# Optimization experiments

Measured on AMD Instinct MI355X. Metric: run time of the kernel, lower is better.

Reference implementation:

```python
import jax, jax.numpy as jnp
import numpy as np

NPOINT = 2048
NSAMPLE = 16
LEAKY = 0.1
BN_EPS = 1e-5


def square_distance(src, dst):
    # src [B,S,3], dst [B,N,3] -> [B,S,N] squared euclidean
    d = -2.0 * jnp.einsum('bsc,bnc->bsn', src, dst)
    d = d + jnp.sum(src * src, -1)[:, :, None]
    d = d + jnp.sum(dst * dst, -1)[:, None, :]
    return d


def furthest_point_sample(xyz, npoint):
    # xyz [B,N,3] -> idx [B,npoint]; matches pointnet2 CUDA (seed = index 0)
    B, N, _ = xyz.shape

    def step(carry, _):
        dist, far = carry  # dist [B,N], far [B]
        centroid = jnp.take_along_axis(xyz, far[:, None, None], axis=1)  # [B,1,3]
        d = jnp.sum((xyz - centroid) ** 2, axis=-1)
        dist = jnp.minimum(dist, d)
        nxt = jnp.argmax(dist, axis=-1).astype(jnp.int32)
        return (dist, nxt), far

    init = (jnp.full((B, N), 1e10, xyz.dtype), jnp.zeros((B,), jnp.int32))
    _, idxs = jax.lax.scan(step, init, None, length=npoint)
    return idxs.T  # [B, npoint]


def _gather_nbrs(p, i):
    # p [N,C], i [S,K] -> [S,K,C]
    return p[i]


gather_group = jax.vmap(_gather_nbrs)


def conv_bn_lrelu(x, W, g, b):
    # x [B,Cin,S,K], W [Cout,Cin]; 1x1 conv + train-mode BatchNorm2d + LeakyReLU
    y = jnp.einsum('oc,bcsk->bosk', W, x)
    mean = jnp.mean(y, axis=(0, 2, 3), keepdims=True)
    var = jnp.var(y, axis=(0, 2, 3), keepdims=True)
    y = (y - mean) * jax.lax.rsqrt(var + BN_EPS)
    y = y * g[None, :, None, None] + b[None, :, None, None]
    return jnp.where(y > 0, y, LEAKY * y)


def setup_inputs() -> dict:
    key = jax.random.key(0)
    ks = jax.random.split(key, 5)
    B, N, D = 4, 8192, 64
    return {
        'xyz': jax.random.normal(ks[0], (B, 3, N), jnp.float32),
        'points': jax.random.normal(ks[1], (B, D, N), jnp.float32),
        'conv0_w': jax.random.normal(ks[2], (64, 67), jnp.float32) * 0.05,
        'conv1_w': jax.random.normal(ks[3], (64, 64), jnp.float32) * 0.05,
        'conv2_w': jax.random.normal(ks[4], (128, 64), jnp.float32) * 0.05,
        'bn0_g': jnp.ones((64,), jnp.float32),
        'bn0_b': jnp.zeros((64,), jnp.float32),
        'bn1_g': jnp.ones((64,), jnp.float32),
        'bn1_b': jnp.zeros((64,), jnp.float32),
        'bn2_g': jnp.ones((128,), jnp.float32),
        'bn2_b': jnp.zeros((128,), jnp.float32),
    }


def reference(xyz, points, conv0_w, conv1_w, conv2_w,
              bn0_g, bn0_b, bn1_g, bn1_b, bn2_g, bn2_b):
    xyz_t = jnp.transpose(xyz, (0, 2, 1))      # [B,N,3]
    pts_t = jnp.transpose(points, (0, 2, 1))   # [B,N,D]

    fps_idx = furthest_point_sample(xyz_t, NPOINT)                       # [B,S]
    new_xyz = jnp.take_along_axis(xyz_t, fps_idx[:, :, None], axis=1)    # [B,S,3]

    sqrd = square_distance(new_xyz, xyz_t)                               # [B,S,N]
    _, idx = jax.lax.top_k(-sqrd, NSAMPLE)                               # [B,S,K]

    grouped_xyz = gather_group(xyz_t, idx)                               # [B,S,K,3]
    grouped_norm = grouped_xyz - new_xyz[:, :, None, :]
    grouped_pts = gather_group(pts_t, idx)                               # [B,S,K,D]
    new_points = jnp.concatenate([grouped_norm, grouped_pts], axis=-1)   # [B,S,K,D+3]
    new_points = jnp.transpose(new_points, (0, 3, 1, 2))                 # [B,D+3,S,K]

    for W, g, b in ((conv0_w, bn0_g, bn0_b), (conv1_w, bn1_g, bn1_b),
                    (conv2_w, bn2_g, bn2_b)):
        new_points = conv_bn_lrelu(new_points, W, g, b)

    feat = jnp.max(new_points, axis=-1)                                  # [B,128,S]
    return jnp.transpose(new_xyz, (0, 2, 1)), feat, fps_idx
```

## Files before the change

### kernel.cpp

```cpp
#include <hip/hip_runtime.h>
#include <hip/hip_bf16.h>

#define BB 4
#define NP 8192
#define SS 2048
#define KK 16
#define DD 64
#define NN (BB*SS*KK)
#define HEATERS 128

typedef float vf2 __attribute__((ext_vector_type(2)));

#if defined(__has_builtin)
#if __has_builtin(__builtin_amdgcn_permlane16_swap) && __has_builtin(__builtin_amdgcn_permlane32_swap)
#define HAVE_PERMLANE_SWAP 1
#endif
#endif

__device__ __forceinline__ float wave_max_f32(float v) {
  int x;
  x = __builtin_amdgcn_update_dpp(0, __float_as_int(v), 0xB1, 0xF, 0xF, true);
  v = fmaxf(v, __int_as_float(x));
  x = __builtin_amdgcn_update_dpp(0, __float_as_int(v), 0x4E, 0xF, 0xF, true);
  v = fmaxf(v, __int_as_float(x));
  x = __builtin_amdgcn_update_dpp(0, __float_as_int(v), 0x141, 0xF, 0xF, true);
  v = fmaxf(v, __int_as_float(x));
  x = __builtin_amdgcn_update_dpp(0, __float_as_int(v), 0x140, 0xF, 0xF, true);
  v = fmaxf(v, __int_as_float(x));
#ifdef HAVE_PERMLANE_SWAP
  {
    unsigned u = __float_as_uint(v);
    auto r16 = __builtin_amdgcn_permlane16_swap(u, u, false, false);
    v = fmaxf(__uint_as_float(r16[0]), __uint_as_float(r16[1]));
    unsigned u2 = __float_as_uint(v);
    auto r32 = __builtin_amdgcn_permlane32_swap(u2, u2, false, false);
    v = fmaxf(__uint_as_float(r32[0]), __uint_as_float(r32[1]));
  }
#else
  x = __builtin_amdgcn_ds_swizzle(__float_as_int(v), 0x401F);
  v = fmaxf(v, __int_as_float(x));
  v = fmaxf(v, __shfl_xor(v, 32, 64));
#endif
  return v;
}

__global__ __launch_bounds__(512) void fps_kernel(
    const float* __restrict__ xyz, float* __restrict__ newXyz,
    float* __restrict__ out, int* __restrict__ done)
{
  const int t = threadIdx.x;

  if (blockIdx.x >= BB) {
    float a0 = 1.0f, a1 = 1.1f, a2 = 1.2f, a3 = 1.3f;
    const float bm = 1.000001f, cm = 1e-7f;
    for (;;) {
      for (int k = 0; k < 1024; k++) {
        a0 = __builtin_fmaf(a0, bm, cm);
        a1 = __builtin_fmaf(a1, bm, cm);
        a2 = __builtin_fmaf(a2, bm, cm);
        a3 = __builtin_fmaf(a3, bm, cm);
      }
      if (__hip_atomic_load(done, __ATOMIC_RELAXED, __HIP_MEMORY_SCOPE_AGENT) >= BB)
        break;
    }
    if (a0 == 123.456f && a1 == 2.f && a2 == 3.f && a3 == 4.f)
      ((volatile int*)done)[1] = 1;
    return;
  }

  const int b = blockIdx.x;
  const float* xb = xyz + (size_t)b * 3 * NP;

  __shared__ float lx[NP], ly[NP], lz[NP];
  __shared__ int   wis[SS];
  __shared__ unsigned long long swin[3];

  vf2 px[8], py[8], pz[8], dist[8];
  const int i0 = t << 4;
#pragma unroll
  for (int h = 0; h < 8; h++) {
    int i = i0 + (h << 1);
    vf2 x = *(const vf2*)(xb + i);
    vf2 y = *(const vf2*)(xb + NP + i);
    vf2 z = *(const vf2*)(xb + 2 * NP + i);
    px[h] = x; py[h] = y; pz[h] = z;
    dist[h] = (vf2){1e10f, 1e10f};
    *(vf2*)(lx + i) = x; *(vf2*)(ly + i) = y; *(vf2*)(lz + i) = z;
  }
  if (t == 0) { wis[0] = 0; swin[0] = 0; swin[1] = 0; swin[2] = 0; }
  __syncthreads();

  float cx = lx[0], cy = ly[0], cz = lz[0];

  for (int it = 1; it < SS; ++it) {
    vf2 c2x = {cx, cx}, c2y = {cy, cy}, c2z = {cz, cz};
    vf2 lb = {-1.0f, -1.0f};
    {
#pragma clang fp contract(off)
#pragma unroll
      for (int h = 0; h < 8; h++) {
        vf2 dx = px[h] - c2x;
        vf2 dy = py[h] - c2y;
        vf2 dz = pz[h] - c2z;
        vf2 d  = (dx * dx + dy * dy) + dz * dz;
        vf2 dm = __builtin_elementwise_min(dist[h], d);
        dist[h] = dm;
        lb = __builtin_elementwise_max(lb, dm);
      }
    }
    float lbest = fmaxf(lb.x, lb.y);
    float Vw = wave_max_f32(lbest);
    int q = it % 3;
    if (lbest == Vw) {
      unsigned mi = 0u;
#pragma unroll
      for (int h = 7; h >= 0; h--) {
        unsigned base = (unsigned)(i0 + (h << 1));
        if (dist[h].y == Vw) mi = base + 1;
        if (dist[h].x == Vw) mi = base;
      }
      unsigned long long pk =
          ((unsigned long long)__float_as_uint(Vw) << 32) | (unsigned)(~mi);
      atomicMax(&swin[q], pk);
    }
    __syncthreads();
    unsigned long long pkf = swin[q];
    int ii = (int)(~((unsigned)pkf));
    if (t == 0) { wis[it] = ii; swin[(q + 2) % 3] = 0; }
    cx = lx[ii]; cy = ly[ii]; cz = lz[ii];
  }
  __syncthreads();

  float* outX = out;
  float* outI = out + 24576 + 1048576;
  for (int s = t; s < SS; s += 512) {
    int iw = wis[s];
    float x = lx[iw], y = ly[iw], z = lz[iw];
    size_t qq = (size_t)(b * SS + s);
    newXyz[qq * 3 + 0] = x;
    newXyz[qq * 3 + 1] = y;
    newXyz[qq * 3 + 2] = z;
    outX[(b * 3 + 0) * SS + s] = x;
    outX[(b * 3 + 1) * SS + s] = y;
    outX[(b * 3 + 2) * SS + s] = z;
    outI[b * SS + s] = (float)iw;
  }
  if (t == 0)
    __hip_atomic_fetch_add(done, 1, __ATOMIC_RELEASE, __HIP_MEMORY_SCOPE_AGENT);
}

__global__ __launch_bounds__(256) void knn_kernel(
    const float* __restrict__ xyz, const float* __restrict__ newXyz,
    int* __restrict__ knnIdx)
{
  const int t = threadIdx.x, w = t >> 6, l = t & 63;
  const int q = blockIdx.x * 4 + w;
  const int b = q >> 11;
  const float* xb = xyz + (size_t)b * 3 * NP;
  float qx = newXyz[q * 3], qy = newXyz[q * 3 + 1], qz = newXyz[q * 3 + 2];
  float ss = __fadd_rn(__fadd_rn(__fmul_rn(qx, qx), __fmul_rn(qy, qy)), __fmul_rn(qz, qz));
  float kd[16]; int ki[16];
#pragma unroll
  for (int j = 0; j < 16; j++) { kd[j] = __builtin_inff(); ki[j] = 0x7fffffff; }

  for (int m = 0; m < 32; m++) {
    int i = (m << 8) + (l << 2);
    float4 xv = *(const float4*)(xb + i);
    float4 yv = *(const float4*)(xb + NP + i);
    float4 zv = *(const float4*)(xb + 2 * NP + i);
#pragma unroll
    for (int c = 0; c < 4; c++) {
      float x = (c == 0) ? xv.x : (c == 1) ? xv.y : (c == 2) ? xv.z : xv.w;
      float y = (c == 0) ? yv.x : (c == 1) ? yv.y : (c == 2) ? yv.z : yv.w;
      float z = (c == 0) ? zv.x : (c == 1) ? zv.y : (c == 2) ? zv.z : zv.w;
      float dot = __fadd_rn(__fadd_rn(__fmul_rn(x, qx), __fmul_rn(y, qy)), __fmul_rn(z, qz));
      float nn  = __fadd_rn(__fadd_rn(__fmul_rn(x, x), __fmul_rn(y, y)), __fmul_rn(z, z));
      float d   = __fadd_rn(__fadd_rn(__fmul_rn(-2.0f, dot), ss), nn);
      if (d < kd[15]) {
        kd[15] = d; ki[15] = i + c;
#pragma unroll
        for (int jj = 15; jj >= 1; jj--) {
          if (kd[jj] < kd[jj - 1]) {
            float td = kd[jj]; kd[jj] = kd[jj - 1]; kd[jj - 1] = td;
            int   ti = ki[jj]; ki[jj] = ki[jj - 1]; ki[jj - 1] = ti;
          }
        }
      }
    }
  }

  __shared__ float sd[4 * 64 * 17];
  __shared__ int   sx[4 * 64 * 17];
  int base = (w * 64 + l) * 17;
#pragma unroll
  for (int j = 0; j < 16; j++) { sd[base + j] = kd[j]; sx[base + j] = ki[j]; }
  __syncthreads();

  int cur = 0; int outIdx = 0;
#pragma unroll 1
  for (int r = 0; r < 16; r++) {
    float hv = (cur < 16) ? sd[base + cur] : __builtin_inff();
    int   hi = (cur < 16) ? sx[base + cur] : 0x7fffffff;
    int   hl = l;
#pragma unroll
    for (int m2 = 1; m2 < 64; m2 <<= 1) {
      float ov = __shfl_xor(hv, m2, 64);
      int   oi = __shfl_xor(hi, m2, 64);
      int   ol = __shfl_xor(hl, m2, 64);
      if (ov < hv || (ov == hv && oi < hi)) { hv = ov; hi = oi; hl = ol; }
    }
    if (l == hl) cur++;
    if (l == r) outIdx = hi;
  }
  if (l < 16) knnIdx[q * 16 + l] = outIdx;
}

__global__ __launch_bounds__(256) void conv0_kernel(
    const float* __restrict__ xyz, const float* __restrict__ points,
    const float* __restrict__ newXyz, const int* __restrict__ knnIdx,
    const float* __restrict__ W, float* __restrict__ Y)
{
  int n = blockIdx.x * 256 + threadIdx.x;
  int b = n >> 15;
  int q = n >> 4;
  int ip = knnIdx[n];
  const float* xb = xyz + (size_t)b * 3 * NP;
  float x[67];
  x[0] = xb[ip]          - newXyz[q * 3 + 0];
  x[1] = xb[NP + ip]     - newXyz[q * 3 + 1];
  x[2] = xb[2 * NP + ip] - newXyz[q * 3 + 2];
  const float* pb = points + (size_t)b * DD * NP + ip;
#pragma unroll 8
  for (int d0 = 0; d0 < DD; d0++)
    x[3 + d0] = pb[(size_t)d0 * NP];
#pragma unroll 1
  for (int o = 0; o < 64; o += 4) {
    float a0 = 0.f, a1 = 0.f, a2 = 0.f, a3 = 0.f;
#pragma unroll
    for (int c = 0; c < 67; c++) {
      float xv = x[c];
      a0 = fmaf(W[(o + 0) * 67 + c], xv, a0);
      a1 = fmaf(W[(o + 1) * 67 + c], xv, a1);
      a2 = fmaf(W[(o + 2) * 67 + c], xv, a2);
      a3 = fmaf(W[(o + 3) * 67 + c], xv, a3);
    }
    Y[(size_t)(o + 0) * NN + n] = a0;
    Y[(size_t)(o + 1) * NN + n] = a1;
    Y[(size_t)(o + 2) * NN + n] = a2;
    Y[(size_t)(o + 3) * NN + n] = a3;
  }
}

template <int CIN, int COUT>
__global__ __launch_bounds__(256) void conv_bn_kernel(
    const float* __restrict__ X, const float* __restrict__ W,
    const float* __restrict__ stats, const float* __restrict__ g,
    const float* __restrict__ bt, float* __restrict__ Y)
{
  __shared__ vf2 sss[CIN];
  if (threadIdx.x < CIN) {
    int c = threadIdx.x;
    float mean = stats[c * 2] * (1.0f / NN);
    float var  = stats[c * 2 + 1] * (1.0f / NN) - mean * mean;
    float inv  = rsqrtf(var + 1e-5f);
    float sc = inv * g[c];
    float sh = bt[c] - mean * sc;
    sss[c] = (vf2){sc, sh};
  }
  __syncthreads();
  int n = blockIdx.x * 256 + threadIdx.x;
  float x[CIN];
#pragma unroll
  for (int c = 0; c < CIN; c++) x[c] = X[(size_t)c * NN + n];
#pragma unroll
  for (int c = 0; c < CIN; c++) {
    vf2 p = sss[c];
    float v = fmaf(x[c], p.x, p.y);
    x[c] = v > 0.0f ? v : 0.1f * v;
  }
#pragma unroll 1
  for (int o = 0; o < COUT; o += 4) {
    float a0 = 0.f, a1 = 0.f, a2 = 0.f, a3 = 0.f;
#pragma unroll
    for (int c = 0; c < CIN; c++) {
      float xv = x[c];
      a0 = fmaf(W[(o + 0) * CIN + c], xv, a0);
      a1 = fmaf(W[(o + 1) * CIN + c], xv, a1);
      a2 = fmaf(W[(o + 2) * CIN + c], xv, a2);
      a3 = fmaf(W[(o + 3) * CIN + c], xv, a3);
    }
    Y[(size_t)(o + 0) * NN + n] = a0;
    Y[(size_t)(o + 1) * NN + n] = a1;
    Y[(size_t)(o + 2) * NN + n] = a2;
    Y[(size_t)(o + 3) * NN + n] = a3;
  }
}

__global__ __launch_bounds__(256) void stats_kernel(
    const float* __restrict__ Y, float* __restrict__ stats)
{
  int c = blockIdx.y;
  int base = blockIdx.x * 4096 + threadIdx.x;
  const float* yc = Y + (size_t)c * NN;
  float s1 = 0.f, s2 = 0.f;
#pragma unroll
  for (int j = 0; j < 16; j++) {
    float v = yc[base + j * 256];
    s1 += v; s2 = fmaf(v, v, s2);
  }
#pragma unroll
  for (int m = 1; m < 64; m <<= 1) {
    s1 += __shfl_xor(s1, m, 64);
    s2 += __shfl_xor(s2, m, 64);
  }
  __shared__ float r1[4], r2[4];
  int w = threadIdx.x >> 6;
  if ((threadIdx.x & 63) == 0) { r1[w] = s1; r2[w] = s2; }
  __syncthreads();
  if (threadIdx.x == 0) {
    float t1 = r1[0] + r1[1] + r1[2] + r1[3];
    float t2 = r2[0] + r2[1] + r2[2] + r2[3];
    atomicAdd(&stats[c * 2], t1);
    atomicAdd(&stats[c * 2 + 1], t2);
  }
}

__global__ __launch_bounds__(256) void maxk_kernel(
    const float* __restrict__ X, const float* __restrict__ stats,
    const float* __restrict__ g, const float* __restrict__ bt,
    float* __restrict__ out)
{
  int m = blockIdx.x * 256 + threadIdx.x;
  int s = m & 2047;
  int o = (m >> 11) & 127;
  int b = m >> 18;
  float mean = stats[o * 2] * (1.0f / NN);
  float var  = stats[o * 2 + 1] * (1.0f / NN) - mean * mean;
  float inv  = rsqrtf(var + 1e-5f);
  float sc = inv * g[o];
  float sh = bt[o] - mean * sc;
  const float4* p = (const float4*)(X + (size_t)o * NN + ((size_t)((b << 11) + s) << 4));
  float mx = -__builtin_inff();
#pragma unroll
  for (int j = 0; j < 4; j++) {
    float4 v4 = p[j];
    float a = fmaf(v4.x, sc, sh); a = a > 0.f ? a : 0.1f * a;
    float b2 = fmaf(v4.y, sc, sh); b2 = b2 > 0.f ? b2 : 0.1f * b2;
    float c = fmaf(v4.z, sc, sh); c = c > 0.f ? c : 0.1f * c;
    float d = fmaf(v4.w, sc, sh); d = d > 0.f ? d : 0.1f * d;
    mx = fmaxf(mx, fmaxf(fmaxf(a, b2), fmaxf(c, d)));
  }
  out[24576 + (size_t)((b << 7) + o) * SS + s] = mx;
}

extern "C" void kernel_launch(void* const* d_in, const int* in_sizes, int n_in,
                              void* d_out, int out_size, void* d_ws, size_t ws_size,
                              hipStream_t stream) {
  const float* xyz    = (const float*)d_in[0];
  const float* points = (const float*)d_in[1];
  const float* w0 = (const float*)d_in[2];
  const float* w1 = (const float*)d_in[3];
  const float* w2 = (const float*)d_in[4];
  const float* g0 = (const float*)d_in[5];
  const float* b0 = (const float*)d_in[6];
  const float* g1 = (const float*)d_in[7];
  const float* b1 = (const float*)d_in[8];
  const float* g2 = (const float*)d_in[9];
  const float* b2 = (const float*)d_in[10];
  float* out = (float*)d_out;

  float* wsf    = (float*)d_ws;
  float* newXyz = wsf;
  int*   knnIdx = (int*)(wsf + 24576);
  float* stats0 = wsf + 155648;
  float* stats1 = wsf + 155904;
  float* stats2 = wsf + 156160;
  int*   done   = (int*)(wsf + 157440);
  float* Xa     = wsf + 160000;
  float* Xb     = wsf + 8941824;

  hipMemsetAsync(stats0, 0, 2048 * 4, stream);

  fps_kernel<<<BB + HEATERS, 512, 0, stream>>>(xyz, newXyz, out, done);
  knn_kernel<<<SS * BB / 4, 256, 0, stream>>>(xyz, newXyz, knnIdx);

  conv0_kernel<<<NN / 256, 256, 0, stream>>>(xyz, points, newXyz, knnIdx, w0, Xb);
  stats_kernel<<<dim3(32, 64), 256, 0, stream>>>(Xb, stats0);

  conv_bn_kernel<64, 64><<<NN / 256, 256, 0, stream>>>(Xb, w1, stats0, g0, b0, Xa);
  stats_kernel<<<dim3(32, 64), 256, 0, stream>>>(Xa, stats1);

  conv_bn_kernel<64, 128><<<NN / 256, 256, 0, stream>>>(Xa, w2, stats1, g1, b1, Xb);
  stats_kernel<<<dim3(32, 128), 256, 0, stream>>>(Xb, stats2);

  maxk_kernel<<<(BB * 128 * SS) / 256, 256, 0, stream>>>(Xb, stats2, g2, b2, out);
}
```

Measured before the change: 2.285 ms.

## Overlap KNN with FPS by streaming centroids to spinning worker blocks

The idle heater blocks in the FPS launch become KNN workers. The FPS blocks publish each new centroid to global memory with atomic stores as soon as it is chosen. Workers spin on sentinel-initialised slots, which are set to 0xFF by a memset, and run the top-16 search for each query while FPS is still iterating. This removes the separate KNN kernel launch and hides its cost behind the serial FPS chain. The risks are spin-wait dependence on co-residency of all blocks and extra per-iteration global stores in the FPS critical loop.

```diff
diff --git a/kernel.cpp b/kernel.cpp
--- a/kernel.cpp
+++ b/kernel.cpp
@@ -7,7 +7,7 @@
 #define KK 16
 #define DD 64
 #define NN (BB*SS*KK)
-#define HEATERS 128
+#define WORKERS 251
 
 typedef float vf2 __attribute__((ext_vector_type(2)));
 
@@ -44,36 +44,127 @@
   return v;
 }
 
+#define SENT 0xFFFFFFFFu
+
 __global__ __launch_bounds__(512) void fps_kernel(
     const float* __restrict__ xyz, float* __restrict__ newXyz,
-    float* __restrict__ out, int* __restrict__ done)
+    float* __restrict__ out, int* __restrict__ done, int* __restrict__ knnIdx)
 {
+  __shared__ __align__(16) char smem[106528];
   const int t = threadIdx.x;
 
   if (blockIdx.x >= BB) {
+    const int w = t >> 6, l = t & 63;
+    float* sd = (float*)smem;
+    int*   sx = (int*)(smem + 34816);
+    const int base = (w * 64 + l) * 17;
+    float hacc = 0.0f;
+    const unsigned gw = (blockIdx.x - BB) * 8 + (unsigned)w;
+
+    for (unsigned q = gw; q < (unsigned)(BB * SS); q += WORKERS * 8) {
+      const int b = q >> 11;
+      const float* xb = xyz + (size_t)b * 3 * NP;
+      const unsigned* nxz = (const unsigned*)newXyz + (size_t)q * 3;
+      float qx, qy, qz;
+      {
+        float h0 = 1.0f, h1 = 1.1f, h2 = 1.2f, h3 = 1.3f;
+        for (;;) {
+          unsigned ux = __hip_atomic_load(nxz + 0, __ATOMIC_RELAXED, __HIP_MEMORY_SCOPE_AGENT);
+          unsigned uy = __hip_atomic_load(nxz + 1, __ATOMIC_RELAXED, __HIP_MEMORY_SCOPE_AGENT);
+          unsigned uz = __hip_atomic_load(nxz + 2, __ATOMIC_RELAXED, __HIP_MEMORY_SCOPE_AGENT);
+          if (ux != SENT && uy != SENT && uz != SENT) {
+            qx = __uint_as_float(ux); qy = __uint_as_float(uy); qz = __uint_as_float(uz);
+            break;
+          }
+#pragma unroll
+          for (int k2 = 0; k2 < 16; k2++) {
+            h0 = __builtin_fmaf(h0, 1.000001f, 1e-7f);
+            h1 = __builtin_fmaf(h1, 1.000001f, 1e-7f);
+            h2 = __builtin_fmaf(h2, 1.000001f, 1e-7f);
+            h3 = __builtin_fmaf(h3, 1.000001f, 1e-7f);
+          }
+        }
+        hacc += h0 + h1 + h2 + h3;
+      }
+
+      float ssq = __fadd_rn(__fadd_rn(__fmul_rn(qx, qx), __fmul_rn(qy, qy)), __fmul_rn(qz, qz));
+      float kd[16]; int ki[16];
+#pragma unroll
+      for (int j = 0; j < 16; j++) { kd[j] = __builtin_inff(); ki[j] = 0x7fffffff; }
+
+      for (int m = 0; m < 32; m++) {
+        int i = (m << 8) + (l << 2);
+        float4 xv = *(const float4*)(xb + i);
+        float4 yv = *(const float4*)(xb + NP + i);
+        float4 zv = *(const float4*)(xb + 2 * NP + i);
+#pragma unroll
+        for (int c = 0; c < 4; c++) {
+          float x = (c == 0) ? xv.x : (c == 1) ? xv.y : (c == 2) ? xv.z : xv.w;
+          float y = (c == 0) ? yv.x : (c == 1) ? yv.y : (c == 2) ? yv.z : yv.w;
+          float z = (c == 0) ? zv.x : (c == 1) ? zv.y : (c == 2) ? zv.z : zv.w;
+          float dot = __fadd_rn(__fadd_rn(__fmul_rn(x, qx), __fmul_rn(y, qy)), __fmul_rn(z, qz));
+          float nn  = __fadd_rn(__fadd_rn(__fmul_rn(x, x), __fmul_rn(y, y)), __fmul_rn(z, z));
+          float d   = __fadd_rn(__fadd_rn(__fmul_rn(-2.0f, dot), ssq), nn);
+          if (d < kd[15]) {
+            kd[15] = d; ki[15] = i + c;
+#pragma unroll
+            for (int jj = 15; jj >= 1; jj--) {
+              if (kd[jj] < kd[jj - 1]) {
+                float td = kd[jj]; kd[jj] = kd[jj - 1]; kd[jj - 1] = td;
+                int   ti = ki[jj]; ki[jj] = ki[jj - 1]; ki[jj - 1] = ti;
+              }
+            }
+          }
+        }
+      }
+
+#pragma unroll
+      for (int j = 0; j < 16; j++) { sd[base + j] = kd[j]; sx[base + j] = ki[j]; }
+
+      int cur = 0; int outIdx = 0;
+#pragma unroll 1
+      for (int r = 0; r < 16; r++) {
+        float hv = (cur < 16) ? sd[base + cur] : __builtin_inff();
+        int   hi = (cur < 16) ? sx[base + cur] : 0x7fffffff;
+        int   hl = l;
+#pragma unroll
+        for (int m2 = 1; m2 < 64; m2 <<= 1) {
+          float ov = __shfl_xor(hv, m2, 64);
+          int   oi = __shfl_xor(hi, m2, 64);
+          int   ol = __shfl_xor(hl, m2, 64);
+          if (ov < hv || (ov == hv && oi < hi)) { hv = ov; hi = oi; hl = ol; }
+        }
+        if (l == hl) cur++;
+        if (l == r) outIdx = hi;
+      }
+      if (l < 16) knnIdx[q * 16 + l] = outIdx;
+    }
+
     float a0 = 1.0f, a1 = 1.1f, a2 = 1.2f, a3 = 1.3f;
-    const float bm = 1.000001f, cm = 1e-7f;
     for (;;) {
       for (int k = 0; k < 1024; k++) {
-        a0 = __builtin_fmaf(a0, bm, cm);
-        a1 = __builtin_fmaf(a1, bm, cm);
-        a2 = __builtin_fmaf(a2, bm, cm);
-        a3 = __builtin_fmaf(a3, bm, cm);
+        a0 = __builtin_fmaf(a0, 1.000001f, 1e-7f);
+        a1 = __builtin_fmaf(a1, 1.000001f, 1e-7f);
+        a2 = __builtin_fmaf(a2, 1.000001f, 1e-7f);
+        a3 = __builtin_fmaf(a3, 1.000001f, 1e-7f);
       }
       if (__hip_atomic_load(done, __ATOMIC_RELAXED, __HIP_MEMORY_SCOPE_AGENT) >= BB)
         break;
     }
-    if (a0 == 123.456f && a1 == 2.f && a2 == 3.f && a3 == 4.f)
+    if (hacc + a0 + a1 + a2 + a3 == 123.456f)
       ((volatile int*)done)[1] = 1;
     return;
   }
 
+  float* lx = (float*)smem;
+  float* ly = (float*)(smem + 32768);
+  float* lz = (float*)(smem + 65536);
+  int*   wis = (int*)(smem + 98304);
+  unsigned long long* swin = (unsigned long long*)(smem + 106496);
+
   const int b = blockIdx.x;
   const float* xb = xyz + (size_t)b * 3 * NP;
-
-  __shared__ float lx[NP], ly[NP], lz[NP];
-  __shared__ int   wis[SS];
-  __shared__ unsigned long long swin[3];
+  unsigned* nxzOut = (unsigned*)newXyz + (size_t)b * SS * 3;
 
   vf2 px[8], py[8], pz[8], dist[8];
   const int i0 = t << 4;
@@ -91,6 +182,11 @@
   __syncthreads();
 
   float cx = lx[0], cy = ly[0], cz = lz[0];
+  if (t == 0) {
+    __hip_atomic_store(nxzOut + 0, __float_as_uint(cx), __ATOMIC_RELAXED, __HIP_MEMORY_SCOPE_AGENT);
+    __hip_atomic_store(nxzOut + 1, __float_as_uint(cy), __ATOMIC_RELAXED, __HIP_MEMORY_SCOPE_AGENT);
+    __hip_atomic_store(nxzOut + 2, __float_as_uint(cz), __ATOMIC_RELAXED, __HIP_MEMORY_SCOPE_AGENT);
+  }
 
   for (int it = 1; it < SS; ++it) {
     vf2 c2x = {cx, cx}, c2y = {cy, cy}, c2z = {cz, cz};
@@ -128,6 +224,12 @@
     int ii = (int)(~((unsigned)pkf));
     if (t == 0) { wis[it] = ii; swin[(q + 2) % 3] = 0; }
     cx = lx[ii]; cy = ly[ii]; cz = lz[ii];
+    if (t == 0) {
+      unsigned* nx = nxzOut + (size_t)it * 3;
+      __hip_atomic_store(nx + 0, __float_as_uint(cx), __ATOMIC_RELAXED, __HIP_MEMORY_SCOPE_AGENT);
+      __hip_atomic_store(nx + 1, __float_as_uint(cy), __ATOMIC_RELAXED, __HIP_MEMORY_SCOPE_AGENT);
+      __hip_atomic_store(nx + 2, __float_as_uint(cz), __ATOMIC_RELAXED, __HIP_MEMORY_SCOPE_AGENT);
+    }
   }
   __syncthreads();
 
@@ -135,84 +237,13 @@
   float* outI = out + 24576 + 1048576;
   for (int s = t; s < SS; s += 512) {
     int iw = wis[s];
-    float x = lx[iw], y = ly[iw], z = lz[iw];
-    size_t qq = (size_t)(b * SS + s);
-    newXyz[qq * 3 + 0] = x;
-    newXyz[qq * 3 + 1] = y;
-    newXyz[qq * 3 + 2] = z;
-    outX[(b * 3 + 0) * SS + s] = x;
-    outX[(b * 3 + 1) * SS + s] = y;
-    outX[(b * 3 + 2) * SS + s] = z;
+    outX[(b * 3 + 0) * SS + s] = lx[iw];
+    outX[(b * 3 + 1) * SS + s] = ly[iw];
+    outX[(b * 3 + 2) * SS + s] = lz[iw];
     outI[b * SS + s] = (float)iw;
   }
   if (t == 0)
     __hip_atomic_fetch_add(done, 1, __ATOMIC_RELEASE, __HIP_MEMORY_SCOPE_AGENT);
-}
-
-__global__ __launch_bounds__(256) void knn_kernel(
-    const float* __restrict__ xyz, const float* __restrict__ newXyz,
-    int* __restrict__ knnIdx)
-{
-  const int t = threadIdx.x, w = t >> 6, l = t & 63;
-  const int q = blockIdx.x * 4 + w;
-  const int b = q >> 11;
-  const float* xb = xyz + (size_t)b * 3 * NP;
-  float qx = newXyz[q * 3], qy = newXyz[q * 3 + 1], qz = newXyz[q * 3 + 2];
-  float ss = __fadd_rn(__fadd_rn(__fmul_rn(qx, qx), __fmul_rn(qy, qy)), __fmul_rn(qz, qz));
-  float kd[16]; int ki[16];
-#pragma unroll
-  for (int j = 0; j < 16; j++) { kd[j] = __builtin_inff(); ki[j] = 0x7fffffff; }
-
-  for (int m = 0; m < 32; m++) {
-    int i = (m << 8) + (l << 2);
-    float4 xv = *(const float4*)(xb + i);
-    float4 yv = *(const float4*)(xb + NP + i);
-    float4 zv = *(const float4*)(xb + 2 * NP + i);
-#pragma unroll
-    for (int c = 0; c < 4; c++) {
-      float x = (c == 0) ? xv.x : (c == 1) ? xv.y : (c == 2) ? xv.z : xv.w;
-      float y = (c == 0) ? yv.x : (c == 1) ? yv.y : (c == 2) ? yv.z : yv.w;
-      float z = (c == 0) ? zv.x : (c == 1) ? zv.y : (c == 2) ? zv.z : zv.w;
-      float dot = __fadd_rn(__fadd_rn(__fmul_rn(x, qx), __fmul_rn(y, qy)), __fmul_rn(z, qz));
-      float nn  = __fadd_rn(__fadd_rn(__fmul_rn(x, x), __fmul_rn(y, y)), __fmul_rn(z, z));
-      float d   = __fadd_rn(__fadd_rn(__fmul_rn(-2.0f, dot), ss), nn);
-      if (d < kd[15]) {
-        kd[15] = d; ki[15] = i + c;
-#pragma unroll
-        for (int jj = 15; jj >= 1; jj--) {
-          if (kd[jj] < kd[jj - 1]) {
-            float td = kd[jj]; kd[jj] = kd[jj - 1]; kd[jj - 1] = td;
-            int   ti = ki[jj]; ki[jj] = ki[jj - 1]; ki[jj - 1] = ti;
-          }
-        }
-      }
-    }
-  }
-
-  __shared__ float sd[4 * 64 * 17];
-  __shared__ int   sx[4 * 64 * 17];
-  int base = (w * 64 + l) * 17;
-#pragma unroll
-  for (int j = 0; j < 16; j++) { sd[base + j] = kd[j]; sx[base + j] = ki[j]; }
-  __syncthreads();
-
-  int cur = 0; int outIdx = 0;
-#pragma unroll 1
-  for (int r = 0; r < 16; r++) {
-    float hv = (cur < 16) ? sd[base + cur] : __builtin_inff();
-    int   hi = (cur < 16) ? sx[base + cur] : 0x7fffffff;
-    int   hl = l;
-#pragma unroll
-    for (int m2 = 1; m2 < 64; m2 <<= 1) {
-      float ov = __shfl_xor(hv, m2, 64);
-      int   oi = __shfl_xor(hi, m2, 64);
-      int   ol = __shfl_xor(hl, m2, 64);
-      if (ov < hv || (ov == hv && oi < hi)) { hv = ov; hi = oi; hl = ol; }
-    }
-    if (l == hl) cur++;
-    if (l == r) outIdx = hi;
-  }
-  if (l < 16) knnIdx[q * 16 + l] = outIdx;
 }
 
 __global__ __launch_bounds__(256) void conv0_kernel(
@@ -380,9 +411,9 @@
   float* Xb     = wsf + 8941824;
 
   hipMemsetAsync(stats0, 0, 2048 * 4, stream);
-
-  fps_kernel<<<BB + HEATERS, 512, 0, stream>>>(xyz, newXyz, out, done);
-  knn_kernel<<<SS * BB / 4, 256, 0, stream>>>(xyz, newXyz, knnIdx);
+  hipMemsetAsync(newXyz, 0xFF, 24576 * 4, stream);
+
+  fps_kernel<<<BB + WORKERS, 512, 0, stream>>>(xyz, newXyz, out, done, knnIdx);
 
   conv0_kernel<<<NN / 256, 256, 0, stream>>>(xyz, points, newXyz, knnIdx, w0, Xb);
   stats_kernel<<<dim3(32, 64), 256, 0, stream>>>(Xb, stats0);
```

Result: slower. 2.534 ms (+10.9%).

## Fuse conv/BN/stats/maxpool tail into one persistent kernel with grid barriers

Applied to the files above, without the earlier changes.

Replaces the seven separate conv, stats and max-pool launches with a single persistent kernel of 512 blocks. A global atomic-counter barrier separates the phases. This is meant to remove launch gaps and kernel boundaries between the dependent stages. It relies on all 512 blocks being co-resident to avoid deadlock, and it adds spin-wait barrier cost.

```diff
diff --git a/kernel.cpp b/kernel.cpp
--- a/kernel.cpp
+++ b/kernel.cpp
@@ -8,6 +8,7 @@
 #define DD 64
 #define NN (BB*SS*KK)
 #define HEATERS 128
+#define TB 512
 
 typedef float vf2 __attribute__((ext_vector_type(2)));
 
@@ -215,142 +216,253 @@
   if (l < 16) knnIdx[q * 16 + l] = outIdx;
 }
 
-__global__ __launch_bounds__(256) void conv0_kernel(
+__device__ __forceinline__ void gbar(int* ctr, int target) {
+  __syncthreads();
+  __threadfence();
+  if (threadIdx.x == 0) {
+    __hip_atomic_fetch_add(ctr, 1, __ATOMIC_RELEASE, __HIP_MEMORY_SCOPE_AGENT);
+    while (__hip_atomic_load(ctr, __ATOMIC_ACQUIRE, __HIP_MEMORY_SCOPE_AGENT) < target)
+      __builtin_amdgcn_s_sleep(1);
+  }
+  __syncthreads();
+  __threadfence();
+}
+
+__global__ __launch_bounds__(256) void tail_kernel(
     const float* __restrict__ xyz, const float* __restrict__ points,
     const float* __restrict__ newXyz, const int* __restrict__ knnIdx,
-    const float* __restrict__ W, float* __restrict__ Y)
+    const float* __restrict__ w0, const float* __restrict__ w1,
+    const float* __restrict__ w2,
+    const float* __restrict__ g0, const float* __restrict__ b0,
+    const float* __restrict__ g1, const float* __restrict__ b1,
+    const float* __restrict__ g2, const float* __restrict__ b2,
+    float* __restrict__ stats0, float* __restrict__ stats1,
+    float* __restrict__ stats2,
+    float* __restrict__ Xa, float* __restrict__ Xb,
+    float* __restrict__ out, int* __restrict__ ctr)
 {
-  int n = blockIdx.x * 256 + threadIdx.x;
-  int b = n >> 15;
-  int q = n >> 4;
-  int ip = knnIdx[n];
-  const float* xb = xyz + (size_t)b * 3 * NP;
-  float x[67];
-  x[0] = xb[ip]          - newXyz[q * 3 + 0];
-  x[1] = xb[NP + ip]     - newXyz[q * 3 + 1];
-  x[2] = xb[2 * NP + ip] - newXyz[q * 3 + 2];
-  const float* pb = points + (size_t)b * DD * NP + ip;
+  const int bk = blockIdx.x, t = threadIdx.x, w = t >> 6;
+  __shared__ vf2 sss[64];
+  __shared__ float r1[4], r2[4];
+
+  {
+    int n = bk * 256 + t;
+    int b = n >> 15;
+    int q = n >> 4;
+    int ip = knnIdx[n];
+    const float* xb = xyz + (size_t)b * 3 * NP;
+    float x[67];
+    x[0] = xb[ip]          - newXyz[q * 3 + 0];
+    x[1] = xb[NP + ip]     - newXyz[q * 3 + 1];
+    x[2] = xb[2 * NP + ip] - newXyz[q * 3 + 2];
+    const float* pb = points + (size_t)b * DD * NP + ip;
 #pragma unroll 8
-  for (int d0 = 0; d0 < DD; d0++)
-    x[3 + d0] = pb[(size_t)d0 * NP];
-#pragma unroll 1
-  for (int o = 0; o < 64; o += 4) {
-    float a0 = 0.f, a1 = 0.f, a2 = 0.f, a3 = 0.f;
-#pragma unroll
-    for (int c = 0; c < 67; c++) {
-      float xv = x[c];
-      a0 = fmaf(W[(o + 0) * 67 + c], xv, a0);
-      a1 = fmaf(W[(o + 1) * 67 + c], xv, a1);
-      a2 = fmaf(W[(o + 2) * 67 + c], xv, a2);
-      a3 = fmaf(W[(o + 3) * 67 + c], xv, a3);
-    }
-    Y[(size_t)(o + 0) * NN + n] = a0;
-    Y[(size_t)(o + 1) * NN + n] = a1;
-    Y[(size_t)(o + 2) * NN + n] = a2;
-    Y[(size_t)(o + 3) * NN + n] = a3;
-  }
-}
-
-template <int CIN, int COUT>
-__global__ __launch_bounds__(256) void conv_bn_kernel(
-    const float* __restrict__ X, const float* __restrict__ W,
-    const float* __restrict__ stats, const float* __restrict__ g,
-    const float* __restrict__ bt, float* __restrict__ Y)
-{
-  __shared__ vf2 sss[CIN];
-  if (threadIdx.x < CIN) {
-    int c = threadIdx.x;
-    float mean = stats[c * 2] * (1.0f / NN);
-    float var  = stats[c * 2 + 1] * (1.0f / NN) - mean * mean;
+    for (int d0 = 0; d0 < DD; d0++)
+      x[3 + d0] = pb[(size_t)d0 * NP];
+#pragma unroll 1
+    for (int o = 0; o < 64; o += 4) {
+      float a0 = 0.f, a1 = 0.f, a2 = 0.f, a3 = 0.f;
+#pragma unroll
+      for (int c = 0; c < 67; c++) {
+        float xv = x[c];
+        a0 = fmaf(w0[(o + 0) * 67 + c], xv, a0);
+        a1 = fmaf(w0[(o + 1) * 67 + c], xv, a1);
+        a2 = fmaf(w0[(o + 2) * 67 + c], xv, a2);
+        a3 = fmaf(w0[(o + 3) * 67 + c], xv, a3);
+      }
+      Xb[(size_t)(o + 0) * NN + n] = a0;
+      Xb[(size_t)(o + 1) * NN + n] = a1;
+      Xb[(size_t)(o + 2) * NN + n] = a2;
+      Xb[(size_t)(o + 3) * NN + n] = a3;
+    }
+  }
+  gbar(ctr, TB);
+
+#pragma unroll 1
+  for (int p = 0; p < 4; ++p) {
+    int vb = p * TB + bk;
+    int c = vb >> 5, xc = vb & 31;
+    const float* yc = Xb + (size_t)c * NN;
+    int base = xc * 4096 + t;
+    float s1 = 0.f, s2 = 0.f;
+#pragma unroll
+    for (int j = 0; j < 16; j++) {
+      float v = yc[base + j * 256];
+      s1 += v; s2 = fmaf(v, v, s2);
+    }
+#pragma unroll
+    for (int m = 1; m < 64; m <<= 1) {
+      s1 += __shfl_xor(s1, m, 64);
+      s2 += __shfl_xor(s2, m, 64);
+    }
+    if ((t & 63) == 0) { r1[w] = s1; r2[w] = s2; }
+    __syncthreads();
+    if (t == 0) {
+      atomicAdd(&stats0[c * 2],     r1[0] + r1[1] + r1[2] + r1[3]);
+      atomicAdd(&stats0[c * 2 + 1], r2[0] + r2[1] + r2[2] + r2[3]);
+    }
+    __syncthreads();
+  }
+  gbar(ctr, 2 * TB);
+
+  {
+    if (t < 64) {
+      int c = t;
+      float mean = stats0[c * 2] * (1.0f / NN);
+      float var  = stats0[c * 2 + 1] * (1.0f / NN) - mean * mean;
+      float inv  = rsqrtf(var + 1e-5f);
+      float sc = inv * g0[c];
+      float sh = b0[c] - mean * sc;
+      sss[c] = (vf2){sc, sh};
+    }
+    __syncthreads();
+    int n = bk * 256 + t;
+    float x[64];
+#pragma unroll
+    for (int c = 0; c < 64; c++) x[c] = Xb[(size_t)c * NN + n];
+#pragma unroll
+    for (int c = 0; c < 64; c++) {
+      vf2 pp = sss[c];
+      float v = fmaf(x[c], pp.x, pp.y);
+      x[c] = v > 0.0f ? v : 0.1f * v;
+    }
+#pragma unroll 1
+    for (int o = 0; o < 64; o += 4) {
+      float a0 = 0.f, a1 = 0.f, a2 = 0.f, a3 = 0.f;
+#pragma unroll
+      for (int c = 0; c < 64; c++) {
+        float xv = x[c];
+        a0 = fmaf(w1[(o + 0) * 64 + c], xv, a0);
+        a1 = fmaf(w1[(o + 1) * 64 + c], xv, a1);
+        a2 = fmaf(w1[(o + 2) * 64 + c], xv, a2);
+        a3 = fmaf(w1[(o + 3) * 64 + c], xv, a3);
+      }
+      Xa[(size_t)(o + 0) * NN + n] = a0;
+      Xa[(size_t)(o + 1) * NN + n] = a1;
+      Xa[(size_t)(o + 2) * NN + n] = a2;
+      Xa[(size_t)(o + 3) * NN + n] = a3;
+    }
+  }
+  gbar(ctr, 3 * TB);
+
+#pragma unroll 1
+  for (int p = 0; p < 4; ++p) {
+    int vb = p * TB + bk;
+    int c = vb >> 5, xc = vb & 31;
+    const float* yc = Xa + (size_t)c * NN;
+    int base = xc * 4096 + t;
+    float s1 = 0.f, s2 = 0.f;
+#pragma unroll
+    for (int j = 0; j < 16; j++) {
+      float v = yc[base + j * 256];
+      s1 += v; s2 = fmaf(v, v, s2);
+    }
+#pragma unroll
+    for (int m = 1; m < 64; m <<= 1) {
+      s1 += __shfl_xor(s1, m, 64);
+      s2 += __shfl_xor(s2, m, 64);
+    }
+    if ((t & 63) == 0) { r1[w] = s1; r2[w] = s2; }
+    __syncthreads();
+    if (t == 0) {
+      atomicAdd(&stats1[c * 2],     r1[0] + r1[1] + r1[2] + r1[3]);
+      atomicAdd(&stats1[c * 2 + 1], r2[0] + r2[1] + r2[2] + r2[3]);
+    }
+    __syncthreads();
+  }
+  gbar(ctr, 4 * TB);
+
+  {
+    if (t < 64) {
+      int c = t;
+      float mean = stats1[c * 2] * (1.0f / NN);
+      float var  = stats1[c * 2 + 1] * (1.0f / NN) - mean * mean;
+      float inv  = rsqrtf(var + 1e-5f);
+      float sc = inv * g1[c];
+      float sh = b1[c] - mean * sc;
+      sss[c] = (vf2){sc, sh};
+    }
+    __syncthreads();
+    int n = bk * 256 + t;
+    float x[64];
+#pragma unroll
+    for (int c = 0; c < 64; c++) x[c] = Xa[(size_t)c * NN + n];
+#pragma unroll
+    for (int c = 0; c < 64; c++) {
+      vf2 pp = sss[c];
+      float v = fmaf(x[c], pp.x, pp.y);
+      x[c] = v > 0.0f ? v : 0.1f * v;
+    }
+#pragma unroll 1
+    for (int o = 0; o < 128; o += 4) {
+      float a0 = 0.f, a1 = 0.f, a2 = 0.f, a3 = 0.f;
+#pragma unroll
+      for (int c = 0; c < 64; c++) {
+        float xv = x[c];
+        a0 = fmaf(w2[(o + 0) * 64 + c], xv, a0);
+        a1 = fmaf(w2[(o + 1) * 64 + c], xv, a1);
+        a2 = fmaf(w2[(o + 2) * 64 + c], xv, a2);
+        a3 = fmaf(w2[(o + 3) * 64 + c], xv, a3);
+      }
+      Xb[(size_t)(o + 0) * NN + n] = a0;
+      Xb[(size_t)(o + 1) * NN + n] = a1;
+      Xb[(size_t)(o + 2) * NN + n] = a2;
+      Xb[(size_t)(o + 3) * NN + n] = a3;
+    }
+  }
+  gbar(ctr, 5 * TB);
+
+#pragma unroll 1
+  for (int p = 0; p < 8; ++p) {
+    int vb = p * TB + bk;
+    int c = vb >> 5, xc = vb & 31;
+    const float* yc = Xb + (size_t)c * NN;
+    int base = xc * 4096 + t;
+    float s1 = 0.f, s2 = 0.f;
+#pragma unroll
+    for (int j = 0; j < 16; j++) {
+      float v = yc[base + j * 256];
+      s1 += v; s2 = fmaf(v, v, s2);
+    }
+#pragma unroll
+    for (int m = 1; m < 64; m <<= 1) {
+      s1 += __shfl_xor(s1, m, 64);
+      s2 += __shfl_xor(s2, m, 64);
+    }
+    if ((t & 63) == 0) { r1[w] = s1; r2[w] = s2; }
+    __syncthreads();
+    if (t == 0) {
+      atomicAdd(&stats2[c * 2],     r1[0] + r1[1] + r1[2] + r1[3]);
+      atomicAdd(&stats2[c * 2 + 1], r2[0] + r2[1] + r2[2] + r2[3]);
+    }
+    __syncthreads();
+  }
+  gbar(ctr, 6 * TB);
+
+#pragma unroll 1
+  for (int p = 0; p < 8; ++p) {
+    int m = (p * TB + bk) * 256 + t;
+    int s = m & 2047;
+    int o = (m >> 11) & 127;
+    int b = m >> 18;
+    float mean = stats2[o * 2] * (1.0f / NN);
+    float var  = stats2[o * 2 + 1] * (1.0f / NN) - mean * mean;
     float inv  = rsqrtf(var + 1e-5f);
-    float sc = inv * g[c];
-    float sh = bt[c] - mean * sc;
-    sss[c] = (vf2){sc, sh};
-  }
-  __syncthreads();
-  int n = blockIdx.x * 256 + threadIdx.x;
-  float x[CIN];
-#pragma unroll
-  for (int c = 0; c < CIN; c++) x[c] = X[(size_t)c * NN + n];
-#pragma unroll
-  for (int c = 0; c < CIN; c++) {
-    vf2 p = sss[c];
-    float v = fmaf(x[c], p.x, p.y);
-    x[c] = v > 0.0f ? v : 0.1f * v;
-  }
-#pragma unroll 1
-  for (int o = 0; o < COUT; o += 4) {
-    float a0 = 0.f, a1 = 0.f, a2 = 0.f, a3 = 0.f;
-#pragma unroll
-    for (int c = 0; c < CIN; c++) {
-      float xv = x[c];
-      a0 = fmaf(W[(o + 0) * CIN + c], xv, a0);
-      a1 = fmaf(W[(o + 1) * CIN + c], xv, a1);
-      a2 = fmaf(W[(o + 2) * CIN + c], xv, a2);
-      a3 = fmaf(W[(o + 3) * CIN + c], xv, a3);
-    }
-    Y[(size_t)(o + 0) * NN + n] = a0;
-    Y[(size_t)(o + 1) * NN + n] = a1;
-    Y[(size_t)(o + 2) * NN + n] = a2;
-    Y[(size_t)(o + 3) * NN + n] = a3;
-  }
-}
-
-__global__ __launch_bounds__(256) void stats_kernel(
-    const float* __restrict__ Y, float* __restrict__ stats)
-{
-  int c = blockIdx.y;
-  int base = blockIdx.x * 4096 + threadIdx.x;
-  const float* yc = Y + (size_t)c * NN;
-  float s1 = 0.f, s2 = 0.f;
-#pragma unroll
-  for (int j = 0; j < 16; j++) {
-    float v = yc[base + j * 256];
-    s1 += v; s2 = fmaf(v, v, s2);
-  }
-#pragma unroll
-  for (int m = 1; m < 64; m <<= 1) {
-    s1 += __shfl_xor(s1, m, 64);
-    s2 += __shfl_xor(s2, m, 64);
-  }
-  __shared__ float r1[4], r2[4];
-  int w = threadIdx.x >> 6;
-  if ((threadIdx.x & 63) == 0) { r1[w] = s1; r2[w] = s2; }
-  __syncthreads();
-  if (threadIdx.x == 0) {
-    float t1 = r1[0] + r1[1] + r1[2] + r1[3];
-    float t2 = r2[0] + r2[1] + r2[2] + r2[3];
-    atomicAdd(&stats[c * 2], t1);
-    atomicAdd(&stats[c * 2 + 1], t2);
-  }
-}
-
-__global__ __launch_bounds__(256) void maxk_kernel(
-    const float* __restrict__ X, const float* __restrict__ stats,
-    const float* __restrict__ g, const float* __restrict__ bt,
-    float* __restrict__ out)
-{
-  int m = blockIdx.x * 256 + threadIdx.x;
-  int s = m & 2047;
-  int o = (m >> 11) & 127;
-  int b = m >> 18;
-  float mean = stats[o * 2] * (1.0f / NN);
-  float var  = stats[o * 2 + 1] * (1.0f / NN) - mean * mean;
-  float inv  = rsqrtf(var + 1e-5f);
-  float sc = inv * g[o];
-  float sh = bt[o] - mean * sc;
-  const float4* p = (const float4*)(X + (size_t)o * NN + ((size_t)((b << 11) + s) << 4));
-  float mx = -__builtin_inff();
-#pragma unroll
-  for (int j = 0; j < 4; j++) {
-    float4 v4 = p[j];
-    float a = fmaf(v4.x, sc, sh); a = a > 0.f ? a : 0.1f * a;
-    float b2 = fmaf(v4.y, sc, sh); b2 = b2 > 0.f ? b2 : 0.1f * b2;
-    float c = fmaf(v4.z, sc, sh); c = c > 0.f ? c : 0.1f * c;
-    float d = fmaf(v4.w, sc, sh); d = d > 0.f ? d : 0.1f * d;
-    mx = fmaxf(mx, fmaxf(fmaxf(a, b2), fmaxf(c, d)));
-  }
-  out[24576 + (size_t)((b << 7) + o) * SS + s] = mx;
+    float sc = inv * g2[o];
+    float sh = b2[o] - mean * sc;
+    const float4* pp = (const float4*)(Xb + (size_t)o * NN + ((size_t)((b << 11) + s) << 4));
+    float mx = -__builtin_inff();
+#pragma unroll
+    for (int j = 0; j < 4; j++) {
+      float4 v4 = pp[j];
+      float a = fmaf(v4.x, sc, sh); a = a > 0.f ? a : 0.1f * a;
+      float b2v = fmaf(v4.y, sc, sh); b2v = b2v > 0.f ? b2v : 0.1f * b2v;
+      float c = fmaf(v4.z, sc, sh); c = c > 0.f ? c : 0.1f * c;
+      float d = fmaf(v4.w, sc, sh); d = d > 0.f ? d : 0.1f * d;
+      mx = fmaxf(mx, fmaxf(fmaxf(a, b2v), fmaxf(c, d)));
+    }
+    out[24576 + (size_t)((b << 7) + o) * SS + s] = mx;
+  }
 }
 
 extern "C" void kernel_launch(void* const* d_in, const int* in_sizes, int n_in,
@@ -376,6 +488,7 @@
   float* stats1 = wsf + 155904;
   float* stats2 = wsf + 156160;
   int*   done   = (int*)(wsf + 157440);
+  int*   ctr    = (int*)(wsf + 157500);
   float* Xa     = wsf + 160000;
   float* Xb     = wsf + 8941824;
 
@@ -383,15 +496,7 @@
 
   fps_kernel<<<BB + HEATERS, 512, 0, stream>>>(xyz, newXyz, out, done);
   knn_kernel<<<SS * BB / 4, 256, 0, stream>>>(xyz, newXyz, knnIdx);
-
-  conv0_kernel<<<NN / 256, 256, 0, stream>>>(xyz, points, newXyz, knnIdx, w0, Xb);
-  stats_kernel<<<dim3(32, 64), 256, 0, stream>>>(Xb, stats0);
-
-  conv_bn_kernel<64, 64><<<NN / 256, 256, 0, stream>>>(Xb, w1, stats0, g0, b0, Xa);
-  stats_kernel<<<dim3(32, 64), 256, 0, stream>>>(Xa, stats1);
-
-  conv_bn_kernel<64, 128><<<NN / 256, 256, 0, stream>>>(Xa, w2, stats1, g1, b1, Xb);
-  stats_kernel<<<dim3(32, 128), 256, 0, stream>>>(Xb, stats2);
-
-  maxk_kernel<<<(BB * 128 * SS) / 256, 256, 0, stream>>>(Xb, stats2, g2, b2, out);
+  tail_kernel<<<TB, 256, 0, stream>>>(xyz, points, newXyz, knnIdx,
+                                      w0, w1, w2, g0, b0, g1, b1, g2, b2,
+                                      stats0, stats1, stats2, Xa, Xb, out, ctr);
 }
```

After: 2.860 ms. 25.1% more time.
